# Kernel tuning notes

Hardware: AMD Instinct MI355X
Metric: run time of the kernel (lower is better)

## Reference

```python
import jax, jax.numpy as jnp
import numpy as np

OUT = 7          # roi_align output size
SR = 2           # sampling_ratio
SCALE = 1.0 / 16.0
T_OUT = 16       # F.interpolate temporal target
EPS = 1e-6


def setup_inputs() -> dict:
    key = jax.random.key(0)
    ks = jax.random.split(key, 12)
    B, Cin, Cout, T, H, W = 1, 1536, 3072, 16, 14, 14
    y = jax.random.normal(ks[0], (B, Cin, T, H, W), jnp.float32)
    x_t = jax.random.normal(ks[1], (B, Cout, T, H, W), jnp.float32)
    # ROIs in 224x224 image coords (spatial_scale = 1/16): one [1,4] box per frame
    x1 = jax.random.uniform(ks[2], (T,), minval=0.0, maxval=112.0)
    y1 = jax.random.uniform(ks[3], (T,), minval=0.0, maxval=112.0)
    x2 = jnp.minimum(x1 + jax.random.uniform(ks[4], (T,), minval=80.0, maxval=112.0), 224.0)
    y2 = jnp.minimum(y1 + jax.random.uniform(ks[5], (T,), minval=80.0, maxval=112.0), 224.0)
    rois = jnp.stack([x1, y1, x2, y2], axis=-1)[:, None, :]  # [T,1,4]
    conv_w = jax.random.normal(ks[6], (Cout, Cin), jnp.float32) * 0.02
    conv_b = jax.random.normal(ks[7], (Cout,), jnp.float32) * 0.02
    gamma = 1.0 + 0.1 * jax.random.normal(ks[8], (Cout,), jnp.float32)
    beta = 0.1 * jax.random.normal(ks[9], (Cout,), jnp.float32)
    run_mean = 0.1 * jax.random.normal(ks[10], (Cout,), jnp.float32)
    run_var = jax.random.uniform(ks[11], (Cout,), minval=0.5, maxval=1.5)
    return dict(y=y, x_t=x_t, rois=rois, conv_w=conv_w, conv_b=conv_b,
                gamma=gamma, beta=beta, run_mean=run_mean, run_var=run_var)


def _bilinear_sample(img, ys, xs):
    # img: [C,H,W]; ys: [Sy]; xs: [Sx] -> [C,Sy,Sx]; torchvision roi_align semantics
    C, H, W = img.shape
    oy = (ys < -1.0) | (ys > H)
    ox = (xs < -1.0) | (xs > W)
    yc = jnp.clip(ys, 0.0, H - 1)
    xc = jnp.clip(xs, 0.0, W - 1)
    y0 = jnp.floor(yc).astype(jnp.int32)
    x0 = jnp.floor(xc).astype(jnp.int32)
    y1i = jnp.minimum(y0 + 1, H - 1)
    x1i = jnp.minimum(x0 + 1, W - 1)
    ly = yc - y0
    lx = xc - x0
    g = lambda yi, xi: img[:, yi[:, None], xi[None, :]]  # [C,Sy,Sx]
    wy0, wy1 = (1.0 - ly)[:, None], ly[:, None]
    wx0, wx1 = (1.0 - lx)[None, :], lx[None, :]
    val = (wy0 * wx0 * g(y0, x0) + wy0 * wx1 * g(y0, x1i)
           + wy1 * wx0 * g(y1i, x0) + wy1 * wx1 * g(y1i, x1i))
    mask = (~oy)[:, None] & (~ox)[None, :]
    return jnp.where(mask[None], val, 0.0)


def _roi_align(feat, boxes):
    # feat: [N,C,H,W]; boxes: [N,4] (one box per image, aligned=False, sampling_ratio=2)
    N, C, H, W = feat.shape
    b = boxes * SCALE
    bx1, by1, bx2, by2 = b[:, 0], b[:, 1], b[:, 2], b[:, 3]
    rw = jnp.maximum(bx2 - bx1, 1.0)
    rh = jnp.maximum(by2 - by1, 1.0)
    bw, bh = rw / OUT, rh / OUT
    # sample positions per bin: (bin + (i+0.5)/SR) * bin_size
    pos = (jnp.arange(OUT, dtype=jnp.float32)[:, None]
           + (jnp.arange(SR, dtype=jnp.float32)[None, :] + 0.5) / SR).reshape(-1)  # [OUT*SR]
    ys = by1[:, None] + pos[None, :] * bh[:, None]
    xs = bx1[:, None] + pos[None, :] * bw[:, None]
    vals = jax.vmap(_bilinear_sample)(feat, ys, xs)  # [N,C,OUT*SR,OUT*SR]
    return vals.reshape(N, C, OUT, SR, OUT, SR).mean(axis=(3, 5))


def reference(y, x_t, rois, conv_w, conv_b, gamma, beta, run_mean, run_var):
    B, Cout, T, Hf, Wf = x_t.shape
    # 1x1x1 Conv3d, stride (1,2,2)
    ys = y[:, :, :, ::2, ::2]                                   # [B,Cin,T,7,7]
    yp = jnp.einsum('bcthw,oc->bothw', ys, conv_w) + conv_b[None, :, None, None, None]
    # BatchNorm3d (eval, eps=1e-6) + GELU (exact)
    inv = gamma / jnp.sqrt(run_var + EPS)
    yp = (yp - run_mean[None, :, None, None, None]) * inv[None, :, None, None, None] \
         + beta[None, :, None, None, None]
    yp = jax.nn.gelu(yp, approximate=False)
    # nearest temporal interpolation to T_OUT (identity when Tin == 16)
    Tin = yp.shape[2]
    tidx = (jnp.arange(T_OUT) * Tin) // T_OUT
    yp = yp[:, :, tidx]                                          # [B,Cout,16,7,7]
    # fusion branch: roi_align over (B*T) frames
    ff = jnp.transpose(x_t, (0, 2, 1, 3, 4)).reshape(B * T, Cout, Hf, Wf)
    boxes = rois[:, 0, :]                                        # [T,4]
    mr = _roi_align(ff, boxes)                                   # [B*T,Cout,7,7]
    mr = jnp.transpose(mr.reshape(B, T, Cout, OUT, OUT), (0, 2, 1, 3, 4))
    weighted = yp * mr                                           # [B,Cout,16,7,7]
    # per-frame 7x7 scatter-write into zeros, same window logic as the torch loop
    bs = boxes * SCALE
    sxi = jnp.floor(bs[:, 0]).astype(jnp.int32)
    syi = jnp.floor(bs[:, 1]).astype(jnp.int32)
    exi = jnp.ceil(bs[:, 2]).astype(jnp.int32)
    eyi = jnp.ceil(bs[:, 3]).astype(jnp.int32)
    ml = jnp.where(sxi + 7 < 14, sxi, exi - 7)
    mt = jnp.where(syi + 7 < 14, syi, eyi - 7)
    def place(w_t, t_off, l_off):  # w_t: [B,Cout,7,7]
        z = jnp.zeros((B, Cout, Hf, Wf), w_t.dtype)
        return jax.lax.dynamic_update_slice(z, w_t, (0, 0, t_off, l_off))
    new_face = jax.vmap(place, in_axes=(2, 0, 0), out_axes=2)(weighted, mt, ml)
    return new_face + x_t
```

## Files before the change

### kernel.cpp

```cpp
#include <hip/hip_runtime.h>

#define KD 1536
#define ND 3072
#define MD 784
#define TT 16

typedef __attribute__((ext_vector_type(8))) short short8;
typedef __attribute__((ext_vector_type(4))) float floatx4;

__device__ __forceinline__ unsigned short f2bf(float f) {
    unsigned int x = __float_as_uint(f);
    unsigned int r = (x + 0x7fffu + ((x >> 16) & 1u)) >> 16;
    return (unsigned short)r;
}

__device__ __forceinline__ void gld_lds16(const unsigned short* g, unsigned short* l) {
    __builtin_amdgcn_global_load_lds((const __attribute__((address_space(1))) void*)g,
                                     (__attribute__((address_space(3))) void*)l, 16, 0, 0);
}

__global__ __launch_bounds__(256) void prep_k(const float* __restrict__ y,
                                              const float* __restrict__ conv_w,
                                              unsigned short* __restrict__ Ap,
                                              unsigned short* __restrict__ Bp) {
    __shared__ __align__(16) float sm[64 * 204];
    const int bid = blockIdx.x;
    const int tid = threadIdx.x;

    if (bid < 384) {
        const int t2 = bid / 24, kc = bid % 24;
        for (int i4 = tid; i4 < 64 * 49; i4 += 256) {
            int c = i4 / 49, p4 = i4 % 49;
            float4 v = *(const float4*)(y + (size_t)(kc * 64 + c) * 3136 + t2 * 196 + p4 * 4);
            *(float4*)(&sm[c * 204 + p4 * 4]) = v;
        }
        __syncthreads();
        for (int item = tid; item < 64 * 49; item += 256) {
            int c = item & 63, ij = item >> 6;
            int i = ij / 7, j = ij % 7;
            Ap[(size_t)(t2 * 49 + ij) * KD + kc * 64 + c] =
                f2bf(sm[c * 204 + (2 * i) * 14 + 2 * j]);
        }
    } else {
        size_t base = (size_t)(bid - 384) * 12288;
#pragma unroll
        for (int v = 0; v < 12; ++v) {
            size_t e = base + v * 1024 + tid * 4;
            float4 w4 = *(const float4*)(conv_w + e);
            ushort4 o;
            o.x = f2bf(w4.x); o.y = f2bf(w4.y); o.z = f2bf(w4.z); o.w = f2bf(w4.w);
            *(ushort4*)(Bp + e) = o;
        }
    }
}

__global__ __launch_bounds__(128, 3) void gemm_k(const unsigned short* __restrict__ Ap,
                                                 const unsigned short* __restrict__ Bp,
                                                 const float* __restrict__ cb,
                                                 const float* __restrict__ gm,
                                                 const float* __restrict__ bt,
                                                 const float* __restrict__ rm,
                                                 const float* __restrict__ rv,
                                                 const float* __restrict__ x_t,
                                                 const float* __restrict__ rois,
                                                 float* __restrict__ out) {
    __shared__ __align__(16) float sm[32 * 196];
    __shared__ float wx0s[14], wx1s[14], wy0s[14], wy1s[14];
    __shared__ int x0s[14], x1s[14], y0s[14], y1s[14];

    unsigned short* const smem = (unsigned short*)sm;
    unsigned short* const As0 = smem;
    unsigned short* const As1 = smem + 4096;
    unsigned short* const Bs0 = smem + 8192;
    unsigned short* const Bs1 = smem + 10240;

    const int tid = threadIdx.x;
    const int n0 = blockIdx.x * 32;
    const int t = blockIdx.y;
    const int aRow0 = t * 49;
    const int wv = tid >> 6;
    const int lane = tid & 63;
    const int l15 = lane & 15, quad = lane >> 4;
    const int prow = lane >> 3, pch = lane & 7;
    const int L = pch ^ prow;

    if (tid < 14) {
        float b0 = rois[t * 4 + 0] * 0.0625f, b1 = rois[t * 4 + 1] * 0.0625f;
        float b2 = rois[t * 4 + 2] * 0.0625f, b3 = rois[t * 4 + 3] * 0.0625f;
        float rw = fmaxf(b2 - b0, 1.0f), rh = fmaxf(b3 - b1, 1.0f);
        float bw = rw * (1.0f / 7.0f), bh = rh * (1.0f / 7.0f);
        int p = tid;
        float pos = (float)(p >> 1) + 0.25f + 0.5f * (float)(p & 1);
        float xs = b0 + pos * bw;
        float ysv = b1 + pos * bh;
        bool vx = (xs >= -1.0f && xs <= 14.0f);
        bool vy = (ysv >= -1.0f && ysv <= 14.0f);
        float xc = fminf(fmaxf(xs, 0.0f), 13.0f);
        float yc = fminf(fmaxf(ysv, 0.0f), 13.0f);
        int x0 = (int)floorf(xc), y0 = (int)floorf(yc);
        x0s[p] = x0; y0s[p] = y0;
        x1s[p] = min(x0 + 1, 13); y1s[p] = min(y0 + 1, 13);
        float lx = xc - (float)x0, ly = yc - (float)y0;
        wx0s[p] = vx ? (1.0f - lx) : 0.0f; wx1s[p] = vx ? lx : 0.0f;
        wy0s[p] = vy ? (1.0f - ly) : 0.0f; wy1s[p] = vy ? ly : 0.0f;
    }

    const unsigned short* gA = Ap + (size_t)(aRow0 + wv * 32 + prow) * KD + L * 8;
    const unsigned short* gB = Bp + (size_t)(n0 + wv * 16 + prow) * KD + L * 8;

    auto stage = [&](unsigned short* aB, unsigned short* bB, int kt) {
#pragma unroll
        for (int v = 0; v < 4; ++v)
            gld_lds16(gA + (size_t)v * 8 * KD + kt, aB + wv * 2048 + v * 512);
#pragma unroll
        for (int v = 0; v < 2; ++v)
            gld_lds16(gB + (size_t)v * 8 * KD + kt, bB + wv * 1024 + v * 512);
    };

    floatx4 acc[2][2];
    acc[0][0] = floatx4{0.f, 0.f, 0.f, 0.f};
    acc[0][1] = floatx4{0.f, 0.f, 0.f, 0.f};
    acc[1][0] = floatx4{0.f, 0.f, 0.f, 0.f};
    acc[1][1] = floatx4{0.f, 0.f, 0.f, 0.f};

    stage(As0, Bs0, 0);
    int p = 0;
    for (int kt = 0; kt < KD; kt += 64, p ^= 1) {
        __syncthreads();
        if (kt + 64 < KD)
            stage(p ? As0 : As1, p ? Bs0 : Bs1, kt + 64);
        const unsigned short* Ab = p ? As1 : As0;
        const unsigned short* Bb = p ? Bs1 : Bs0;
#pragma unroll
        for (int ko = 0; ko < 2; ++ko) {
            int ch = ((ko * 4 + quad) ^ (l15 & 7)) * 8;
            short8 a0 = *(const short8*)(Ab + (wv * 32 + l15) * 64 + ch);
            short8 a1 = *(const short8*)(Ab + (wv * 32 + 16 + l15) * 64 + ch);
            short8 b0 = *(const short8*)(Bb + (l15) * 64 + ch);
            short8 b1 = *(const short8*)(Bb + (16 + l15) * 64 + ch);
            acc[0][0] = __builtin_amdgcn_mfma_f32_16x16x32_bf16(a0, b0, acc[0][0], 0, 0, 0);
            acc[0][1] = __builtin_amdgcn_mfma_f32_16x16x32_bf16(a0, b1, acc[0][1], 0, 0, 0);
            acc[1][0] = __builtin_amdgcn_mfma_f32_16x16x32_bf16(a1, b0, acc[1][0], 0, 0, 0);
            acc[1][1] = __builtin_amdgcn_mfma_f32_16x16x32_bf16(a1, b1, acc[1][1], 0, 0, 0);
        }
    }

    __syncthreads();
    for (int i4 = tid; i4 < 32 * 49; i4 += 128) {
        int c = i4 / 49, p4 = i4 % 49;
        float4 xv = *(const float4*)(x_t + (size_t)(n0 + c) * 3136 + t * 196 + p4 * 4);
        *(float4*)(&sm[c * 196 + p4 * 4]) = xv;
    }
    __syncthreads();

#pragma unroll
    for (int ni = 0; ni < 2; ++ni) {
        const int cl = ni * 16 + l15;
        const int n = n0 + cl;
        const float scale = gm[n] / sqrtf(rv[n] + 1e-6f);
        const float shift = (cb[n] - rm[n]) * scale + bt[n];
        const float* base = &sm[cl * 196];
#pragma unroll
        for (int mi = 0; mi < 2; ++mi) {
#pragma unroll
            for (int r = 0; r < 4; ++r) {
                const int m = wv * 32 + mi * 16 + quad * 4 + r;
                if (m < 49) {
                    const int i = m / 7, j = m % 7;
                    float sum = 0.0f;
#pragma unroll
                    for (int s = 0; s < 2; ++s) {
                        int pp = 2 * i + s;
#pragma unroll
                        for (int u = 0; u < 2; ++u) {
                            int q = 2 * j + u;
                            float v00 = base[y0s[pp] * 14 + x0s[q]];
                            float v01 = base[y0s[pp] * 14 + x1s[q]];
                            float v10 = base[y1s[pp] * 14 + x0s[q]];
                            float v11 = base[y1s[pp] * 14 + x1s[q]];
                            sum += wy0s[pp] * (wx0s[q] * v00 + wx1s[q] * v01) +
                                   wy1s[pp] * (wx0s[q] * v10 + wx1s[q] * v11);
                        }
                    }
                    const float mrv = 0.25f * sum;
                    const float v = acc[mi][ni][r] * scale + shift;
                    const float g = 0.5f * v * (1.0f + erff(v * 0.70710678118654752f));
                    acc[mi][ni][r] = g * mrv;
                }
            }
        }
    }
    __syncthreads();

    float b0 = rois[t * 4 + 0] * 0.0625f, b1 = rois[t * 4 + 1] * 0.0625f;
    float b2 = rois[t * 4 + 2] * 0.0625f, b3 = rois[t * 4 + 3] * 0.0625f;
    int sxi = (int)floorf(b0), syi = (int)floorf(b1);
    int exi = (int)ceilf(b2), eyi = (int)ceilf(b3);
    int ml = (sxi + 7 < 14) ? sxi : exi - 7;
    int mt = (syi + 7 < 14) ? syi : eyi - 7;
    ml = min(max(ml, 0), 7);
    mt = min(max(mt, 0), 7);

#pragma unroll
    for (int ni = 0; ni < 2; ++ni) {
        const int cl = ni * 16 + l15;
#pragma unroll
        for (int mi = 0; mi < 2; ++mi) {
#pragma unroll
            for (int r = 0; r < 4; ++r) {
                const int m = wv * 32 + mi * 16 + quad * 4 + r;
                if (m < 49) {
                    const int i = m / 7, j = m % 7;
                    sm[cl * 196 + (mt + i) * 14 + (ml + j)] += acc[mi][ni][r];
                }
            }
        }
    }
    __syncthreads();

    for (int i4 = tid; i4 < 32 * 49; i4 += 128) {
        int c = i4 / 49, p4 = i4 % 49;
        float4 xv = *(const float4*)(&sm[c * 196 + p4 * 4]);
        size_t e0 = (size_t)(n0 + c) * 3136 + t * 196 + p4 * 4;
        *(float4*)(out + e0) = xv;
    }
}

extern "C" void kernel_launch(void* const* d_in, const int* in_sizes, int n_in,
                              void* d_out, int out_size, void* d_ws, size_t ws_size,
                              hipStream_t stream) {
    const float* y = (const float*)d_in[0];
    const float* x_t = (const float*)d_in[1];
    const float* rois = (const float*)d_in[2];
    const float* conv_w = (const float*)d_in[3];
    const float* cb = (const float*)d_in[4];
    const float* gm = (const float*)d_in[5];
    const float* bt = (const float*)d_in[6];
    const float* rm = (const float*)d_in[7];
    const float* rv = (const float*)d_in[8];
    float* out = (float*)d_out;

    char* ws = (char*)d_ws;
    unsigned short* Ap = (unsigned short*)ws;
    unsigned short* Bp = (unsigned short*)(ws + 2555904);

    prep_k<<<768, 256, 0, stream>>>(y, conv_w, Ap, Bp);
    gemm_k<<<dim3(ND / 32, TT), 128, 0, stream>>>(Ap, Bp, cb, gm, bt, rm, rv, x_t, rois, out);
}
```

Baseline: 161.3 us.

## Load GEMM operands straight into registers and widen the N tile to 64

The GEMM kernel no longer stages A and B through LDS with async global-to-LDS copies and per-step barriers. Each wave now loads bf16 fragments directly from global memory into registers, double-buffered across K steps. The block's N tile grows from 32 to 64 channels, giving 8 accumulators per wave, and occupancy hint drops from 3 to 2 blocks per SIMD. The prep kernel now reads only the even spatial rows needed for the strided 7x7 subsample. The intent is to remove LDS traffic and barrier stalls and to increase reuse per block, at the cost of uncoalesced per-lane global loads, more register pressure and fewer blocks in the grid.

```diff
diff --git a/kernel.cpp b/kernel.cpp
--- a/kernel.cpp
+++ b/kernel.cpp
@@ -2,7 +2,6 @@
 
 #define KD 1536
 #define ND 3072
-#define MD 784
 #define TT 16
 
 typedef __attribute__((ext_vector_type(8))) short short8;
@@ -14,32 +13,29 @@
     return (unsigned short)r;
 }
 
-__device__ __forceinline__ void gld_lds16(const unsigned short* g, unsigned short* l) {
-    __builtin_amdgcn_global_load_lds((const __attribute__((address_space(1))) void*)g,
-                                     (__attribute__((address_space(3))) void*)l, 16, 0, 0);
-}
+#define MF(a, b, c) __builtin_amdgcn_mfma_f32_16x16x32_bf16(a, b, c, 0, 0, 0)
 
 __global__ __launch_bounds__(256) void prep_k(const float* __restrict__ y,
                                               const float* __restrict__ conv_w,
                                               unsigned short* __restrict__ Ap,
                                               unsigned short* __restrict__ Bp) {
-    __shared__ __align__(16) float sm[64 * 204];
+    __shared__ float smA[64 * 99];
     const int bid = blockIdx.x;
     const int tid = threadIdx.x;
 
     if (bid < 384) {
         const int t2 = bid / 24, kc = bid % 24;
-        for (int i4 = tid; i4 < 64 * 49; i4 += 256) {
-            int c = i4 / 49, p4 = i4 % 49;
-            float4 v = *(const float4*)(y + (size_t)(kc * 64 + c) * 3136 + t2 * 196 + p4 * 4);
-            *(float4*)(&sm[c * 204 + p4 * 4]) = v;
+        for (int f = tid; f < 64 * 98; f += 256) {
+            int c = f / 98, rp = f % 98;
+            int row = (rp / 14) * 2, col = rp % 14;
+            smA[c * 99 + rp] = y[(size_t)(kc * 64 + c) * 3136 + t2 * 196 + row * 14 + col];
         }
         __syncthreads();
         for (int item = tid; item < 64 * 49; item += 256) {
             int c = item & 63, ij = item >> 6;
             int i = ij / 7, j = ij % 7;
             Ap[(size_t)(t2 * 49 + ij) * KD + kc * 64 + c] =
-                f2bf(sm[c * 204 + (2 * i) * 14 + 2 * j]);
+                f2bf(smA[c * 99 + i * 14 + 2 * j]);
         }
     } else {
         size_t base = (size_t)(bid - 384) * 12288;
@@ -54,7 +50,7 @@
     }
 }
 
-__global__ __launch_bounds__(128, 3) void gemm_k(const unsigned short* __restrict__ Ap,
+__global__ __launch_bounds__(128, 2) void gemm_k(const unsigned short* __restrict__ Ap,
                                                  const unsigned short* __restrict__ Bp,
                                                  const float* __restrict__ cb,
                                                  const float* __restrict__ gm,
@@ -64,25 +60,17 @@
                                                  const float* __restrict__ x_t,
                                                  const float* __restrict__ rois,
                                                  float* __restrict__ out) {
-    __shared__ __align__(16) float sm[32 * 196];
+    __shared__ __align__(16) float sm[64 * 196];
     __shared__ float wx0s[14], wx1s[14], wy0s[14], wy1s[14];
     __shared__ int x0s[14], x1s[14], y0s[14], y1s[14];
 
-    unsigned short* const smem = (unsigned short*)sm;
-    unsigned short* const As0 = smem;
-    unsigned short* const As1 = smem + 4096;
-    unsigned short* const Bs0 = smem + 8192;
-    unsigned short* const Bs1 = smem + 10240;
-
     const int tid = threadIdx.x;
-    const int n0 = blockIdx.x * 32;
+    const int n0 = blockIdx.x * 64;
     const int t = blockIdx.y;
     const int aRow0 = t * 49;
     const int wv = tid >> 6;
     const int lane = tid & 63;
     const int l15 = lane & 15, quad = lane >> 4;
-    const int prow = lane >> 3, pch = lane & 7;
-    const int L = pch ^ prow;
 
     if (tid < 14) {
         float b0 = rois[t * 4 + 0] * 0.0625f, b1 = rois[t * 4 + 1] * 0.0625f;
@@ -105,48 +93,53 @@
         wy0s[p] = vy ? (1.0f - ly) : 0.0f; wy1s[p] = vy ? ly : 0.0f;
     }
 
-    const unsigned short* gA = Ap + (size_t)(aRow0 + wv * 32 + prow) * KD + L * 8;
-    const unsigned short* gB = Bp + (size_t)(n0 + wv * 16 + prow) * KD + L * 8;
-
-    auto stage = [&](unsigned short* aB, unsigned short* bB, int kt) {
-#pragma unroll
-        for (int v = 0; v < 4; ++v)
-            gld_lds16(gA + (size_t)v * 8 * KD + kt, aB + wv * 2048 + v * 512);
-#pragma unroll
-        for (int v = 0; v < 2; ++v)
-            gld_lds16(gB + (size_t)v * 8 * KD + kt, bB + wv * 1024 + v * 512);
-    };
-
-    floatx4 acc[2][2];
-    acc[0][0] = floatx4{0.f, 0.f, 0.f, 0.f};
-    acc[0][1] = floatx4{0.f, 0.f, 0.f, 0.f};
-    acc[1][0] = floatx4{0.f, 0.f, 0.f, 0.f};
-    acc[1][1] = floatx4{0.f, 0.f, 0.f, 0.f};
-
-    stage(As0, Bs0, 0);
-    int p = 0;
-    for (int kt = 0; kt < KD; kt += 64, p ^= 1) {
-        __syncthreads();
-        if (kt + 64 < KD)
-            stage(p ? As0 : As1, p ? Bs0 : Bs1, kt + 64);
-        const unsigned short* Ab = p ? As1 : As0;
-        const unsigned short* Bb = p ? Bs1 : Bs0;
-#pragma unroll
-        for (int ko = 0; ko < 2; ++ko) {
-            int ch = ((ko * 4 + quad) ^ (l15 & 7)) * 8;
-            short8 a0 = *(const short8*)(Ab + (wv * 32 + l15) * 64 + ch);
-            short8 a1 = *(const short8*)(Ab + (wv * 32 + 16 + l15) * 64 + ch);
-            short8 b0 = *(const short8*)(Bb + (l15) * 64 + ch);
-            short8 b1 = *(const short8*)(Bb + (16 + l15) * 64 + ch);
-            acc[0][0] = __builtin_amdgcn_mfma_f32_16x16x32_bf16(a0, b0, acc[0][0], 0, 0, 0);
-            acc[0][1] = __builtin_amdgcn_mfma_f32_16x16x32_bf16(a0, b1, acc[0][1], 0, 0, 0);
-            acc[1][0] = __builtin_amdgcn_mfma_f32_16x16x32_bf16(a1, b0, acc[1][0], 0, 0, 0);
-            acc[1][1] = __builtin_amdgcn_mfma_f32_16x16x32_bf16(a1, b1, acc[1][1], 0, 0, 0);
-        }
-    }
-
-    __syncthreads();
-    for (int i4 = tid; i4 < 32 * 49; i4 += 128) {
+    const short8* pa0 = (const short8*)(Ap + (size_t)(aRow0 + wv * 32 + l15) * KD) + quad;
+    const short8* pa1 = pa0 + 2 * KD;
+    const short8* pb0 = (const short8*)(Bp + (size_t)(n0 + l15) * KD) + quad;
+    const short8* pb1 = pb0 + 2 * KD;
+    const short8* pb2 = pb0 + 4 * KD;
+    const short8* pb3 = pb0 + 6 * KD;
+
+    floatx4 acc[2][4] = {};
+
+    short8 xa00, xa01, xa10, xa11, xb00, xb01, xb10, xb11, xb20, xb21, xb30, xb31;
+    short8 ya00, ya01, ya10, ya11, yb00, yb01, yb10, yb11, yb20, yb21, yb30, yb31;
+
+#define LDSET(P, T) { const int kk = (T) * 8;                              \
+        P##a00 = pa0[kk]; P##a01 = pa0[kk + 4];                            \
+        P##a10 = pa1[kk]; P##a11 = pa1[kk + 4];                            \
+        P##b00 = pb0[kk]; P##b01 = pb0[kk + 4];                            \
+        P##b10 = pb1[kk]; P##b11 = pb1[kk + 4];                            \
+        P##b20 = pb2[kk]; P##b21 = pb2[kk + 4];                            \
+        P##b30 = pb3[kk]; P##b31 = pb3[kk + 4]; }
+
+#define FMASET(P)                                                          \
+        acc[0][0] = MF(P##a00, P##b00, acc[0][0]);                         \
+        acc[0][1] = MF(P##a00, P##b10, acc[0][1]);                         \
+        acc[0][2] = MF(P##a00, P##b20, acc[0][2]);                         \
+        acc[0][3] = MF(P##a00, P##b30, acc[0][3]);                         \
+        acc[1][0] = MF(P##a10, P##b00, acc[1][0]);                         \
+        acc[1][1] = MF(P##a10, P##b10, acc[1][1]);                         \
+        acc[1][2] = MF(P##a10, P##b20, acc[1][2]);                         \
+        acc[1][3] = MF(P##a10, P##b30, acc[1][3]);                         \
+        acc[0][0] = MF(P##a01, P##b01, acc[0][0]);                         \
+        acc[0][1] = MF(P##a01, P##b11, acc[0][1]);                         \
+        acc[0][2] = MF(P##a01, P##b21, acc[0][2]);                         \
+        acc[0][3] = MF(P##a01, P##b31, acc[0][3]);                         \
+        acc[1][0] = MF(P##a11, P##b01, acc[1][0]);                         \
+        acc[1][1] = MF(P##a11, P##b11, acc[1][1]);                         \
+        acc[1][2] = MF(P##a11, P##b21, acc[1][2]);                         \
+        acc[1][3] = MF(P##a11, P##b31, acc[1][3]);
+
+    LDSET(x, 0)
+    for (int it2 = 0; it2 < 12; ++it2) {
+        LDSET(y, 2 * it2 + 1)
+        FMASET(x)
+        if (it2 < 11) { LDSET(x, 2 * it2 + 2) }
+        FMASET(y)
+    }
+
+    for (int i4 = tid; i4 < 64 * 49; i4 += 128) {
         int c = i4 / 49, p4 = i4 % 49;
         float4 xv = *(const float4*)(x_t + (size_t)(n0 + c) * 3136 + t * 196 + p4 * 4);
         *(float4*)(&sm[c * 196 + p4 * 4]) = xv;
@@ -154,7 +147,7 @@
     __syncthreads();
 
 #pragma unroll
-    for (int ni = 0; ni < 2; ++ni) {
+    for (int ni = 0; ni < 4; ++ni) {
         const int cl = ni * 16 + l15;
         const int n = n0 + cl;
         const float scale = gm[n] / sqrtf(rv[n] + 1e-6f);
@@ -202,7 +195,7 @@
     mt = min(max(mt, 0), 7);
 
 #pragma unroll
-    for (int ni = 0; ni < 2; ++ni) {
+    for (int ni = 0; ni < 4; ++ni) {
         const int cl = ni * 16 + l15;
 #pragma unroll
         for (int mi = 0; mi < 2; ++mi) {
@@ -218,7 +211,7 @@
     }
     __syncthreads();
 
-    for (int i4 = tid; i4 < 32 * 49; i4 += 128) {
+    for (int i4 = tid; i4 < 64 * 49; i4 += 128) {
         int c = i4 / 49, p4 = i4 % 49;
         float4 xv = *(const float4*)(&sm[c * 196 + p4 * 4]);
         size_t e0 = (size_t)(n0 + c) * 3136 + t * 196 + p4 * 4;
@@ -245,5 +238,5 @@
     unsigned short* Bp = (unsigned short*)(ws + 2555904);
 
     prep_k<<<768, 256, 0, stream>>>(y, conv_w, Ap, Bp);
-    gemm_k<<<dim3(ND / 32, TT), 128, 0, stream>>>(Ap, Bp, cb, gm, bt, rm, rv, x_t, rois, out);
-}
+    gemm_k<<<dim3(ND / 64, TT), 128, 0, stream>>>(Ap, Bp, cb, gm, bt, rm, rv, x_t, rois, out);
+}
```

Result: slower. 203.6 us (+26.2%).

## Shrink GEMM LDS footprint to single buffer and read x_t directly from global

Applied to the files above, without the earlier changes.

The GEMM kernel drops LDS double buffering and the full 32x196 x_t tile, staging one A/B buffer and a small 49x33 result tile instead. The roi_align bilinear taps now read x_t straight from global memory, and the final pass adds the placed 7x7 window while streaming x_t to the output. Occupancy bounds rise from 3 to 6 blocks per SM, and the prep kernel loads only the even rows it needs. The single buffer adds a second barrier per k-step and removes load/compute overlap. The roi taps become scattered global loads instead of LDS reads.

```diff
diff --git a/kernel.cpp b/kernel.cpp
--- a/kernel.cpp
+++ b/kernel.cpp
@@ -2,7 +2,6 @@
 
 #define KD 1536
 #define ND 3072
-#define MD 784
 #define TT 16
 
 typedef __attribute__((ext_vector_type(8))) short short8;
@@ -19,27 +18,29 @@
                                      (__attribute__((address_space(3))) void*)l, 16, 0, 0);
 }
 
+#define MF(a, b, c) __builtin_amdgcn_mfma_f32_16x16x32_bf16(a, b, c, 0, 0, 0)
+
 __global__ __launch_bounds__(256) void prep_k(const float* __restrict__ y,
                                               const float* __restrict__ conv_w,
                                               unsigned short* __restrict__ Ap,
                                               unsigned short* __restrict__ Bp) {
-    __shared__ __align__(16) float sm[64 * 204];
+    __shared__ float smA[64 * 99];
     const int bid = blockIdx.x;
     const int tid = threadIdx.x;
 
     if (bid < 384) {
         const int t2 = bid / 24, kc = bid % 24;
-        for (int i4 = tid; i4 < 64 * 49; i4 += 256) {
-            int c = i4 / 49, p4 = i4 % 49;
-            float4 v = *(const float4*)(y + (size_t)(kc * 64 + c) * 3136 + t2 * 196 + p4 * 4);
-            *(float4*)(&sm[c * 204 + p4 * 4]) = v;
+        for (int f = tid; f < 64 * 98; f += 256) {
+            int c = f / 98, rp = f % 98;
+            int row = (rp / 14) * 2, col = rp % 14;
+            smA[c * 99 + rp] = y[(size_t)(kc * 64 + c) * 3136 + t2 * 196 + row * 14 + col];
         }
         __syncthreads();
         for (int item = tid; item < 64 * 49; item += 256) {
             int c = item & 63, ij = item >> 6;
             int i = ij / 7, j = ij % 7;
             Ap[(size_t)(t2 * 49 + ij) * KD + kc * 64 + c] =
-                f2bf(sm[c * 204 + (2 * i) * 14 + 2 * j]);
+                f2bf(smA[c * 99 + i * 14 + 2 * j]);
         }
     } else {
         size_t base = (size_t)(bid - 384) * 12288;
@@ -54,7 +55,7 @@
     }
 }
 
-__global__ __launch_bounds__(128, 3) void gemm_k(const unsigned short* __restrict__ Ap,
+__global__ __launch_bounds__(128, 6) void gemm_k(const unsigned short* __restrict__ Ap,
                                                  const unsigned short* __restrict__ Bp,
                                                  const float* __restrict__ cb,
                                                  const float* __restrict__ gm,
@@ -64,15 +65,13 @@
                                                  const float* __restrict__ x_t,
                                                  const float* __restrict__ rois,
                                                  float* __restrict__ out) {
-    __shared__ __align__(16) float sm[32 * 196];
+    __shared__ __align__(16) float smf[3136];
     __shared__ float wx0s[14], wx1s[14], wy0s[14], wy1s[14];
     __shared__ int x0s[14], x1s[14], y0s[14], y1s[14];
 
-    unsigned short* const smem = (unsigned short*)sm;
-    unsigned short* const As0 = smem;
-    unsigned short* const As1 = smem + 4096;
-    unsigned short* const Bs0 = smem + 8192;
-    unsigned short* const Bs1 = smem + 10240;
+    unsigned short* const As = (unsigned short*)smf;
+    unsigned short* const Bs = (unsigned short*)smf + 4096;
+    float* const Wl = smf;
 
     const int tid = threadIdx.x;
     const int n0 = blockIdx.x * 32;
@@ -108,13 +107,13 @@
     const unsigned short* gA = Ap + (size_t)(aRow0 + wv * 32 + prow) * KD + L * 8;
     const unsigned short* gB = Bp + (size_t)(n0 + wv * 16 + prow) * KD + L * 8;
 
-    auto stage = [&](unsigned short* aB, unsigned short* bB, int kt) {
+    auto stage = [&](int kt) {
 #pragma unroll
         for (int v = 0; v < 4; ++v)
-            gld_lds16(gA + (size_t)v * 8 * KD + kt, aB + wv * 2048 + v * 512);
+            gld_lds16(gA + (size_t)v * 8 * KD + kt, As + wv * 2048 + v * 512);
 #pragma unroll
         for (int v = 0; v < 2; ++v)
-            gld_lds16(gB + (size_t)v * 8 * KD + kt, bB + wv * 1024 + v * 512);
+            gld_lds16(gB + (size_t)v * 8 * KD + kt, Bs + wv * 1024 + v * 512);
     };
 
     floatx4 acc[2][2];
@@ -123,35 +122,25 @@
     acc[1][0] = floatx4{0.f, 0.f, 0.f, 0.f};
     acc[1][1] = floatx4{0.f, 0.f, 0.f, 0.f};
 
-    stage(As0, Bs0, 0);
-    int p = 0;
-    for (int kt = 0; kt < KD; kt += 64, p ^= 1) {
+    stage(0);
+    for (int kt = 0; kt < KD; kt += 64) {
+        __syncthreads();
+#pragma unroll
+        for (int ko = 0; ko < 2; ++ko) {
+            int ch = ((ko * 4 + quad) ^ (l15 & 7)) * 8;
+            short8 a0 = *(const short8*)(As + (wv * 32 + l15) * 64 + ch);
+            short8 a1 = *(const short8*)(As + (wv * 32 + 16 + l15) * 64 + ch);
+            short8 b0 = *(const short8*)(Bs + (l15) * 64 + ch);
+            short8 b1 = *(const short8*)(Bs + (16 + l15) * 64 + ch);
+            acc[0][0] = MF(a0, b0, acc[0][0]);
+            acc[0][1] = MF(a0, b1, acc[0][1]);
+            acc[1][0] = MF(a1, b0, acc[1][0]);
+            acc[1][1] = MF(a1, b1, acc[1][1]);
+        }
         __syncthreads();
         if (kt + 64 < KD)
-            stage(p ? As0 : As1, p ? Bs0 : Bs1, kt + 64);
-        const unsigned short* Ab = p ? As1 : As0;
-        const unsigned short* Bb = p ? Bs1 : Bs0;
-#pragma unroll
-        for (int ko = 0; ko < 2; ++ko) {
-            int ch = ((ko * 4 + quad) ^ (l15 & 7)) * 8;
-            short8 a0 = *(const short8*)(Ab + (wv * 32 + l15) * 64 + ch);
-            short8 a1 = *(const short8*)(Ab + (wv * 32 + 16 + l15) * 64 + ch);
-            short8 b0 = *(const short8*)(Bb + (l15) * 64 + ch);
-            short8 b1 = *(const short8*)(Bb + (16 + l15) * 64 + ch);
-            acc[0][0] = __builtin_amdgcn_mfma_f32_16x16x32_bf16(a0, b0, acc[0][0], 0, 0, 0);
-            acc[0][1] = __builtin_amdgcn_mfma_f32_16x16x32_bf16(a0, b1, acc[0][1], 0, 0, 0);
-            acc[1][0] = __builtin_amdgcn_mfma_f32_16x16x32_bf16(a1, b0, acc[1][0], 0, 0, 0);
-            acc[1][1] = __builtin_amdgcn_mfma_f32_16x16x32_bf16(a1, b1, acc[1][1], 0, 0, 0);
-        }
-    }
-
-    __syncthreads();
-    for (int i4 = tid; i4 < 32 * 49; i4 += 128) {
-        int c = i4 / 49, p4 = i4 % 49;
-        float4 xv = *(const float4*)(x_t + (size_t)(n0 + c) * 3136 + t * 196 + p4 * 4);
-        *(float4*)(&sm[c * 196 + p4 * 4]) = xv;
-    }
-    __syncthreads();
+            stage(kt + 64);
+    }
 
 #pragma unroll
     for (int ni = 0; ni < 2; ++ni) {
@@ -159,7 +148,7 @@
         const int n = n0 + cl;
         const float scale = gm[n] / sqrtf(rv[n] + 1e-6f);
         const float shift = (cb[n] - rm[n]) * scale + bt[n];
-        const float* base = &sm[cl * 196];
+        const float* gx = x_t + (size_t)(n0 + cl) * 3136 + t * 196;
 #pragma unroll
         for (int mi = 0; mi < 2; ++mi) {
 #pragma unroll
@@ -174,10 +163,10 @@
 #pragma unroll
                         for (int u = 0; u < 2; ++u) {
                             int q = 2 * j + u;
-                            float v00 = base[y0s[pp] * 14 + x0s[q]];
-                            float v01 = base[y0s[pp] * 14 + x1s[q]];
-                            float v10 = base[y1s[pp] * 14 + x0s[q]];
-                            float v11 = base[y1s[pp] * 14 + x1s[q]];
+                            float v00 = gx[y0s[pp] * 14 + x0s[q]];
+                            float v01 = gx[y0s[pp] * 14 + x1s[q]];
+                            float v10 = gx[y1s[pp] * 14 + x0s[q]];
+                            float v11 = gx[y1s[pp] * 14 + x1s[q]];
                             sum += wy0s[pp] * (wx0s[q] * v00 + wx1s[q] * v01) +
                                    wy1s[pp] * (wx0s[q] * v10 + wx1s[q] * v11);
                         }
@@ -190,6 +179,20 @@
             }
         }
     }
+
+#pragma unroll
+    for (int ni = 0; ni < 2; ++ni) {
+        const int cl = ni * 16 + l15;
+#pragma unroll
+        for (int mi = 0; mi < 2; ++mi) {
+#pragma unroll
+            for (int r = 0; r < 4; ++r) {
+                const int m = wv * 32 + mi * 16 + quad * 4 + r;
+                if (m < 49)
+                    Wl[m * 33 + cl] = acc[mi][ni][r];
+            }
+        }
+    }
     __syncthreads();
 
     float b0 = rois[t * 4 + 0] * 0.0625f, b1 = rois[t * 4 + 1] * 0.0625f;
@@ -201,28 +204,20 @@
     ml = min(max(ml, 0), 7);
     mt = min(max(mt, 0), 7);
 
-#pragma unroll
-    for (int ni = 0; ni < 2; ++ni) {
-        const int cl = ni * 16 + l15;
-#pragma unroll
-        for (int mi = 0; mi < 2; ++mi) {
-#pragma unroll
-            for (int r = 0; r < 4; ++r) {
-                const int m = wv * 32 + mi * 16 + quad * 4 + r;
-                if (m < 49) {
-                    const int i = m / 7, j = m % 7;
-                    sm[cl * 196 + (mt + i) * 14 + (ml + j)] += acc[mi][ni][r];
-                }
-            }
-        }
-    }
-    __syncthreads();
-
     for (int i4 = tid; i4 < 32 * 49; i4 += 128) {
         int c = i4 / 49, p4 = i4 % 49;
-        float4 xv = *(const float4*)(&sm[c * 196 + p4 * 4]);
         size_t e0 = (size_t)(n0 + c) * 3136 + t * 196 + p4 * 4;
-        *(float4*)(out + e0) = xv;
+        float4 xv = *(const float4*)(x_t + e0);
+        float r4[4] = {xv.x, xv.y, xv.z, xv.w};
+#pragma unroll
+        for (int u = 0; u < 4; ++u) {
+            int pix = p4 * 4 + u;
+            int h = pix / 14, w = pix % 14;
+            int i = h - mt, j = w - ml;
+            if (i >= 0 && i < 7 && j >= 0 && j < 7)
+                r4[u] += Wl[(i * 7 + j) * 33 + c];
+        }
+        *(float4*)(out + e0) = make_float4(r4[0], r4[1], r4[2], r4[3]);
     }
 }
 
```

After: 216.7 us. +34.4%, slower.
